# Performance work log

Hardware: AMD Instinct MI355X
Metric: run time of the kernel (lower is better)

## Reference

```python
import jax, jax.numpy as jnp
import numpy as np
from jax import lax

EPS = 1e-5

def conv3x3(x, w):
    # x: [B,C,H,W], w: [O,C,3,3]
    return lax.conv_general_dilated(x, w, (1, 1), ((1, 1), (1, 1)),
                                    dimension_numbers=("NCHW", "OIHW", "NCHW"))

def convbnrelu(x, w, bn):
    gamma, beta, mean, var = bn  # each [C]
    y = conv3x3(x, w)
    scale = (gamma / jnp.sqrt(var + EPS))[:, None, None]
    shift = (beta - mean * gamma / jnp.sqrt(var + EPS))[:, None, None]
    return jax.nn.relu(y * scale + shift)

def conv1x1(x, w, b):
    # w: [O,C,1,1], b: [O]
    return jnp.einsum("bchw,oc->bohw", x, w[:, :, 0, 0]) + b[:, None, None]

def pam(x, wb, bb, wc, bc, wd, bd, alpha, lfm=None):
    B, C, H, W = x.shape
    N = H * W
    q = conv1x1(x, wb, bb)
    k = conv1x1(x, wc, bc)
    v = conv1x1(x, wd, bd)
    if lfm is not None:  # VFAM: qkv flags all 1 -> multiply q, k, v
        q = q * lfm
        k = k * lfm
        v = v * lfm
    fb = q.reshape(B, -1, N).transpose(0, 2, 1)           # [B,N,Cq]
    fc = k.reshape(B, -1, N)                              # [B,Cq,N]
    attn = jax.nn.softmax(jnp.matmul(fb, fc), axis=-1)    # [B,N,N]
    fd = v.reshape(B, C, N)                               # [B,C,N]
    fe = jnp.matmul(fd, attn.transpose(0, 2, 1)).reshape(B, C, H, W)
    return alpha * fe + x

def cam(x, beta):
    B, C, H, W = x.shape
    N = H * W
    fa = x.reshape(B, C, N)
    attn = jnp.matmul(fa, fa.transpose(0, 2, 1))          # [B,C,C]
    attn = jnp.max(attn, axis=-1, keepdims=True) - attn
    attn = jax.nn.softmax(attn, axis=-1)
    fe = jnp.matmul(attn, fa).reshape(B, C, H, W)
    return beta * fe + x

def setup_inputs() -> dict:
    key = jax.random.key(0)
    ks = iter(jax.random.split(key, 64))
    B, Cin, H, W = 2, 2048, 64, 64
    Cmid = Cin // 4         # 512
    Cq = Cmid // 8          # 64
    nclass = 19

    def bn_pack(C):
        g = jnp.ones((C,)) + 0.1 * jax.random.normal(next(ks), (C,))
        b = 0.1 * jax.random.normal(next(ks), (C,))
        m = 0.1 * jax.random.normal(next(ks), (C,))
        v = jax.random.uniform(next(ks), (C,), minval=0.5, maxval=1.5)
        return jnp.stack([g, b, m, v])  # [4,C]

    def conv_w(O, I, kk):
        return jax.random.normal(next(ks), (O, I, kk, kk)) * (1.0 / np.sqrt(I * kk * kk))

    inp = {
        "x": jax.random.normal(next(ks), (B, Cin, H, W)),
        "loss_factor_map": jax.random.uniform(next(ks), (H, W)),
        "wp1": conv_w(Cmid, Cin, 3), "bnp1": bn_pack(Cmid),
        "wp2": conv_w(Cmid, Cmid, 3), "bnp2": bn_pack(Cmid),
        "wc1": conv_w(Cmid, Cin, 3), "bnc1": bn_pack(Cmid),
        "wc2": conv_w(Cmid, Cmid, 3), "bnc2": bn_pack(Cmid),
        "wv1": conv_w(Cmid, Cin, 3), "bnv1": bn_pack(Cmid),
        "wv2": conv_w(Cmid, Cmid, 3), "bnv2": bn_pack(Cmid),
        "pam_wb": conv_w(Cq, Cmid, 1), "pam_bb": jnp.zeros((Cq,)),
        "pam_wc": conv_w(Cq, Cmid, 1), "pam_bc": jnp.zeros((Cq,)),
        "pam_wd": conv_w(Cmid, Cmid, 1), "pam_bd": jnp.zeros((Cmid,)),
        "pam_alpha": 0.3 * jnp.ones((1,)),
        "cam_beta": 0.3 * jnp.ones((1,)),
        "vfam_wb": conv_w(Cq, Cmid, 1), "vfam_bb": jnp.zeros((Cq,)),
        "vfam_wc": conv_w(Cq, Cmid, 1), "vfam_bc": jnp.zeros((Cq,)),
        "vfam_wd": conv_w(Cmid, Cmid, 1), "vfam_bd": jnp.zeros((Cmid,)),
        "vfam_alpha": 0.3 * jnp.ones((1,)),
        "out_w": conv_w(nclass, Cmid, 1), "out_b": jnp.zeros((nclass,)),
        "p3_w": conv_w(nclass, Cmid, 1), "p3_b": jnp.zeros((nclass,)),
        "c3_w": conv_w(nclass, Cmid, 1), "c3_b": jnp.zeros((nclass,)),
    }
    return inp

def reference(x, loss_factor_map,
              wp1, bnp1, wp2, bnp2, wc1, bnc1, wc2, bnc2, wv1, bnv1, wv2, bnv2,
              pam_wb, pam_bb, pam_wc, pam_bc, pam_wd, pam_bd, pam_alpha,
              cam_beta,
              vfam_wb, vfam_bb, vfam_wc, vfam_bc, vfam_wd, vfam_bd, vfam_alpha,
              out_w, out_b, p3_w, p3_b, c3_w, c3_b):
    lfm = loss_factor_map[None, None, :, :]  # (1,1,H,W)
    # Position branch
    fp = convbnrelu(x, wp1, bnp1)
    fp = pam(fp, pam_wb, pam_bb, pam_wc, pam_bc, pam_wd, pam_bd, pam_alpha)
    fp = convbnrelu(fp, wp2, bnp2)
    # Channel branch
    fc = convbnrelu(x, wc1, bnc1)
    fc = cam(fc, cam_beta)
    fc = convbnrelu(fc, wc2, bnc2)
    # Visual-field branch (qkv_vfa_flag = [1,1,1])
    fv = convbnrelu(x, wv1, bnv1)
    fv = pam(fv, vfam_wb, vfam_bb, vfam_wc, vfam_bc, vfam_wd, vfam_bd, vfam_alpha, lfm=lfm)
    fv = convbnrelu(fv, wv2, bnv2)
    # Fusion + heads (Dropout in eval mode = identity)
    fusion = fp + fc + fv
    fusion_out = conv1x1(fusion, out_w, out_b)
    p_out = conv1x1(fp, p3_w, p3_b)
    c_out = conv1x1(fc, c3_w, c3_b)
    return (fusion_out, p_out, c_out)
```

## Files before the change

### kernel.cpp

```cpp
#include <hip/hip_runtime.h>

typedef unsigned short u16;
typedef short s16x8 __attribute__((ext_vector_type(8)));
typedef u16 u16x8 __attribute__((ext_vector_type(8)));
typedef u16 u16x4 __attribute__((ext_vector_type(4)));
typedef float f32x4 __attribute__((ext_vector_type(4)));

#define DEV __device__ __forceinline__

DEV float bf2f(u16 x) { unsigned v = ((unsigned)x) << 16; float f; __builtin_memcpy(&f, &v, 4); return f; }
DEV u16 f2bf(float f) { unsigned u; __builtin_memcpy(&u, &f, 4); u += 0x7FFFu + ((u >> 16) & 1u); return (u16)(u >> 16); }

DEV void gload16(const u16* g, u16* l) {
  __builtin_amdgcn_global_load_lds((const __attribute__((address_space(1))) void*)g,
                                   (__attribute__((address_space(3))) void*)l, 16, 0, 0);
}

__global__ void detect_dtype(const u16* __restrict__ x, int* __restrict__ flag) {
  int tid = threadIdx.x;
  float mx = 0.f;
  for (int i = tid; i < 4096; i += 256) mx = fmaxf(mx, fabsf(bf2f(x[i])));
  __shared__ float red[4];
  int wave = tid >> 6, lane = tid & 63;
  for (int off = 32; off; off >>= 1) mx = fmaxf(mx, __shfl_xor(mx, off));
  if (lane == 0) red[wave] = mx;
  __syncthreads();
  if (tid == 0) {
    mx = fmaxf(fmaxf(red[0], red[1]), fmaxf(red[2], red[3]));
    *flag = (mx > 1e4f) ? 1 : 0;
  }
}

__global__ void convert_in(const void* __restrict__ src, u16* __restrict__ dst, int n,
                           const int* __restrict__ flag) {
  int i = blockIdx.x * 256 + threadIdx.x;
  if (i >= n) return;
  if (*flag) dst[i] = f2bf(((const float*)src)[i]);
  else       dst[i] = ((const u16*)src)[i];
}

__global__ void bn_prep(const u16* __restrict__ cbn, float* __restrict__ out) {
  int w = blockIdx.x;
  const u16* bn = cbn + w * 2048;
  int c = threadIdx.x;
  float g = bf2f(bn[c]), be = bf2f(bn[512 + c]), m = bf2f(bn[1024 + c]), v = bf2f(bn[1536 + c]);
  float sc = g * rsqrtf(v + 1e-5f);
  out[w * 1024 + c] = sc;
  out[w * 1024 + 512 + c] = be - m * sc;
}

__global__ __launch_bounds__(256) void repack_w3(const void* __restrict__ w, u16* __restrict__ wr,
                                                 int I, int Ishift, const int* __restrict__ flag) {
  const int isF = *flag;
  size_t idx = ((size_t)blockIdx.x * 256 + threadIdx.x) * 8;
  int i0 = (int)(idx & (size_t)(I - 1));
  int t = (int)(idx >> Ishift);
  int o = t / 9, kk = t - o * 9;
  u16x8 v;
  if (isF) {
    const float* f = (const float*)w;
#pragma unroll
    for (int j = 0; j < 8; ++j) v[j] = f2bf(f[((size_t)o * I + i0 + j) * 9 + kk]);
  } else {
    const u16* bsrc = (const u16*)w;
#pragma unroll
    for (int j = 0; j < 8; ++j) v[j] = bsrc[((size_t)o * I + i0 + j) * 9 + kk];
  }
  *(u16x8*)&wr[idx] = v;
}

__global__ __launch_bounds__(256) void pad_nchw(const void* __restrict__ x, u16* __restrict__ xpad,
                                                const int* __restrict__ flag) {
  __shared__ u16 t[64][72];
  const int isF = *flag;
  int c0 = blockIdx.x * 64, h = blockIdx.y, b = blockIdx.z;
  int tid = threadIdx.x;
#pragma unroll
  for (int i = 0; i < 2; ++i) {
    int idx = i * 256 + tid;
    int cc = idx >> 3, ww = (idx & 7) * 8;
    size_t base = (((size_t)(b * 2048 + c0 + cc) * 64) + h) * 64 + ww;
    u16x8 v;
    if (isF) {
      const float* fx = (const float*)x;
#pragma unroll
      for (int j = 0; j < 8; ++j) v[j] = f2bf(fx[base + j]);
    } else {
      v = *(const u16x8*)&((const u16*)x)[base];
    }
    *(u16x8*)&t[cc][ww] = v;
  }
  __syncthreads();
#pragma unroll
  for (int i = 0; i < 2; ++i) {
    int idx = i * 256 + tid;
    int ww = idx >> 3, cc = (idx & 7) * 8;
    u16x8 v;
#pragma unroll
    for (int j = 0; j < 8; ++j) v[j] = t[cc + j][ww];
    *(u16x8*)&xpad[(((size_t)b * 66 + h + 1) * 66 + ww + 1) * 2048 + c0 + cc] = v;
  }
}

__global__ __launch_bounds__(256) void transpose64(const u16* __restrict__ src, u16* __restrict__ dst,
                                                   int R, int C) {
  __shared__ u16 t[64][72];
  int r0 = blockIdx.x * 64, c0 = blockIdx.y * 64;
  const u16* s = src + (size_t)blockIdx.z * R * C;
  u16* d = dst + (size_t)blockIdx.z * R * C;
  int tid = threadIdx.x;
#pragma unroll
  for (int i = 0; i < 2; ++i) {
    int idx = i * 256 + tid;
    int rr = idx >> 3, cc = (idx & 7) * 8;
    u16x8 v = *(const u16x8*)&s[(size_t)(r0 + rr) * C + c0 + cc];
    *(u16x8*)&t[rr][cc] = v;
  }
  __syncthreads();
#pragma unroll
  for (int i = 0; i < 2; ++i) {
    int idx = i * 256 + tid;
    int cc = idx >> 3, rr = (idx & 7) * 8;
    u16x8 v;
#pragma unroll
    for (int j = 0; j < 8; ++j) v[j] = t[rr + j][cc];
    *(u16x8*)&d[(size_t)(c0 + cc) * R + r0 + rr] = v;
  }
}

struct GemmP {
  const u16* A; const u16* B;
  long aBatch, bBatch;
  int M, N, K;
  u16* out; long outBatch; int ldOut;
  const u16* bias;
  const u16* rowscale;
  const u16* residual; long resBatch; int ldRes;
  const u16* alphaPtr;
  float* outF; long outFBatch;
  const u16* B2; const u16* bias2; u16* out2;
};

template <int BM, int BN, int EPI>
__global__ __launch_bounds__(256) void gemm_nt(GemmP p) {
  static_assert(EPI != 2 || BM >= BN, "EPI2 LDS bounce needs BM>=BN");
  __shared__ __align__(16) u16 lsBuf[(BM + BN) * 32];
  u16* lA = lsBuf;
  u16* lB = lsBuf + BM * 32;
  const int tid = threadIdx.x;
  int bz = blockIdx.z;
  const u16* Bsel = p.B;
  const u16* biasSel = p.bias;
  u16* outSel = p.out;
  if (EPI == 0 && p.out2) {
    const int h = gridDim.z >> 1;
    if (bz >= h) { bz -= h; Bsel = p.B2; biasSel = p.bias2; outSel = p.out2; }
  }
  const int m0 = blockIdx.x * BM, n0 = blockIdx.y * BN;
  const u16* A = p.A + (size_t)bz * p.aBatch;
  const u16* Bp = Bsel + (size_t)bz * p.bBatch;
  const int wave = tid >> 6, lane = tid & 63;
  const int quad = lane >> 4, r16 = lane & 15;
  const int wm = (wave >> 1) * (BM / 2), wn = (wave & 1) * (BN / 2);
  constexpr int TM = BM / 32, TN = BN / 32;
  f32x4 acc[TM][TN] = {};
  const int srow = tid >> 2, sch = (tid & 3) * 8;
  const int K = p.K;
  for (int k0 = 0; k0 < K; k0 += 32) {
    u16x8 ra[BM / 64], rb[BN / 64];
#pragma unroll
    for (int i = 0; i < BM / 64; ++i)
      ra[i] = *(const u16x8*)&A[(size_t)(m0 + i * 64 + srow) * K + k0 + sch];
#pragma unroll
    for (int i = 0; i < BN / 64; ++i)
      rb[i] = *(const u16x8*)&Bp[(size_t)(n0 + i * 64 + srow) * K + k0 + sch];
    __syncthreads();
#pragma unroll
    for (int i = 0; i < BM / 64; ++i) *(u16x8*)&lA[i * 2048 + tid * 8] = ra[i];
#pragma unroll
    for (int i = 0; i < BN / 64; ++i) *(u16x8*)&lB[i * 2048 + tid * 8] = rb[i];
    __syncthreads();
    s16x8 av[TM], bv[TN];
#pragma unroll
    for (int t = 0; t < TM; ++t) av[t] = *(const s16x8*)&lA[(wm + t * 16 + r16) * 32 + quad * 8];
#pragma unroll
    for (int t = 0; t < TN; ++t) bv[t] = *(const s16x8*)&lB[(wn + t * 16 + r16) * 32 + quad * 8];
#pragma unroll
    for (int i = 0; i < TM; ++i)
#pragma unroll
      for (int j = 0; j < TN; ++j)
        acc[i][j] = __builtin_amdgcn_mfma_f32_16x16x32_bf16(av[i], bv[j], acc[i][j], 0, 0, 0);
  }
  if constexpr (EPI == 2) {
    float* lsF = (float*)lsBuf;
#pragma unroll
    for (int i = 0; i < TM; ++i) {
      __syncthreads();
#pragma unroll
      for (int j = 0; j < TN; ++j) {
        const int col = wn + j * 16 + r16;
#pragma unroll
        for (int r = 0; r < 4; ++r) {
          const int rowL = (wave >> 1) * 16 + quad * 4 + r;
          lsF[rowL * BN + col] = acc[i][j][r];
        }
      }
      __syncthreads();
      constexpr int PASSES = (32 * BN) / 1024;
#pragma unroll
      for (int pp = 0; pp < PASSES; ++pp) {
        const int lin = (pp * 256 + tid) * 4;
        const int rowL = lin / BN, col = lin & (BN - 1);
        const int gm = m0 + (rowL >> 4) * (BM / 2) + i * 16 + (rowL & 15);
        *(f32x4*)&p.outF[(size_t)bz * p.outFBatch + (size_t)gm * p.ldOut + (n0 + col)] =
            *(const f32x4*)&lsF[lin];
      }
    }
    return;
  }
  float alpha = 0.f;
  if (EPI == 3) alpha = bf2f(p.alphaPtr[0]);
#pragma unroll
  for (int i = 0; i < TM; ++i) {
#pragma unroll
    for (int j = 0; j < TN; ++j) {
      const int nn = n0 + wn + j * 16 + r16;
      float bia = 0.f;
      if ((EPI == 0 || EPI == 1) && biasSel) bia = bf2f(biasSel[nn]);
#pragma unroll
      for (int r = 0; r < 4; ++r) {
        const int mm = m0 + wm + i * 16 + quad * 4 + r;
        float v = acc[i][j][r];
        if (EPI == 0) {
          v += bia;
          if (p.rowscale) v *= bf2f(p.rowscale[mm]);
          outSel[(size_t)bz * p.outBatch + (size_t)mm * p.ldOut + nn] = f2bf(v);
        } else if (EPI == 1) {
          v += bia;
          if (p.rowscale) v *= bf2f(p.rowscale[mm]);
          p.out[(size_t)bz * p.outBatch + (size_t)nn * p.ldOut + mm] = f2bf(v);
        } else {
          float res = bf2f(p.residual[(size_t)bz * p.resBatch + (size_t)mm * p.ldRes + nn]);
          v = alpha * v + res;
          const int py = mm >> 6, px = mm & 63;
          p.out[(size_t)bz * p.outBatch + ((size_t)(py + 1) * 66 + (px + 1)) * p.ldOut + nn] = f2bf(v);
        }
      }
    }
  }
}

struct Conv3P {
  const u16* in[3];
  const u16* wr[3];
  u16* out[3];
  const float* bn;
};

template <int CIN>
__global__ __launch_bounds__(256) void conv3x3_k(Conv3P p) {
  __shared__ u16 lA[4096], lB[4096];
  const int tid = threadIdx.x;
  const int z = blockIdx.z, ci = z >> 1, b = z & 1;
  const int m0 = blockIdx.x * 128, n0 = blockIdx.y * 128;
  const u16* __restrict__ xin = p.in[ci];
  const u16* __restrict__ wr = p.wr[ci];
  const int wave = tid >> 6, lane = tid & 63;
  const int quad = lane >> 4, r16 = lane & 15;
  const int wm = (wave >> 1) * 64, wn = (wave & 1) * 64;
  f32x4 acc[4][4] = {};
  const int srow = tid >> 2, sch = (tid & 3) * 8;
  const int p0 = m0 + srow, p1 = p0 + 64;
  const size_t a0 = (((size_t)b * 66 + (p0 >> 6)) * 66 + (p0 & 63)) * CIN + sch;
  const size_t a1 = (((size_t)b * 66 + (p1 >> 6)) * 66 + (p1 & 63)) * CIN + sch;
  const size_t b0 = ((size_t)(n0 + srow) * 9) * CIN + sch;
  const size_t b1 = ((size_t)(n0 + 64 + srow) * 9) * CIN + sch;
  u16* la0 = &lA[wave * 512];
  u16* la1 = &lA[2048 + wave * 512];
  u16* lb0 = &lB[wave * 512];
  u16* lb1 = &lB[2048 + wave * 512];
  for (int kh = 0; kh < 3; ++kh) {
    for (int kw = 0; kw < 3; ++kw) {
      const size_t soff = ((size_t)kh * 66 + kw) * CIN;
      const size_t woff = (size_t)(kh * 3 + kw) * CIN;
      for (int c = 0; c < CIN; c += 32) {
        __syncthreads();
        gload16(&xin[a0 + soff + c], la0);
        gload16(&xin[a1 + soff + c], la1);
        gload16(&wr[b0 + woff + c], lb0);
        gload16(&wr[b1 + woff + c], lb1);
        __syncthreads();
        s16x8 av[4], bv[4];
#pragma unroll
        for (int t = 0; t < 4; ++t) av[t] = *(const s16x8*)&lA[(wm + t * 16 + r16) * 32 + quad * 8];
#pragma unroll
        for (int t = 0; t < 4; ++t) bv[t] = *(const s16x8*)&lB[(wn + t * 16 + r16) * 32 + quad * 8];
#pragma unroll
        for (int i = 0; i < 4; ++i)
#pragma unroll
          for (int j = 0; j < 4; ++j)
            acc[i][j] = __builtin_amdgcn_mfma_f32_16x16x32_bf16(av[i], bv[j], acc[i][j], 0, 0, 0);
      }
    }
  }
  u16* __restrict__ out = p.out[ci];
  const float* bnS = p.bn + ci * 1024;
#pragma unroll
  for (int i = 0; i < 4; ++i) {
#pragma unroll
    for (int j = 0; j < 4; ++j) {
      const int nn = n0 + wn + j * 16 + r16;
      const float s = bnS[nn], sh = bnS[512 + nn];
#pragma unroll
      for (int r = 0; r < 4; ++r) {
        const int mm = m0 + wm + i * 16 + quad * 4 + r;
        float v = fmaxf(acc[i][j][r] * s + sh, 0.f);
        out[((size_t)b * 4096 + mm) * 512 + nn] = f2bf(v);
      }
    }
  }
}

__global__ __launch_bounds__(256) void softmax4096(const float* __restrict__ S, u16* __restrict__ P) {
  int row = blockIdx.x, tid = threadIdx.x;
  const float* sr = S + (size_t)row * 4096;
  f32x4 v[4];
  float mx = -3.4e38f;
#pragma unroll
  for (int i = 0; i < 4; ++i) {
    v[i] = *(const f32x4*)&sr[(i * 256 + tid) * 4];
    mx = fmaxf(mx, fmaxf(fmaxf(v[i][0], v[i][1]), fmaxf(v[i][2], v[i][3])));
  }
  __shared__ float red[8];
  int wave = tid >> 6, lane = tid & 63;
  for (int off = 32; off; off >>= 1) mx = fmaxf(mx, __shfl_xor(mx, off));
  if (lane == 0) red[wave] = mx;
  __syncthreads();
  mx = fmaxf(fmaxf(red[0], red[1]), fmaxf(red[2], red[3]));
  float sum = 0.f;
#pragma unroll
  for (int i = 0; i < 4; ++i)
#pragma unroll
    for (int j = 0; j < 4; ++j) { float e = __expf(v[i][j] - mx); v[i][j] = e; sum += e; }
  for (int off = 32; off; off >>= 1) sum += __shfl_xor(sum, off);
  if (lane == 0) red[4 + wave] = sum;
  __syncthreads();
  sum = red[4] + red[5] + red[6] + red[7];
  float inv = 1.f / sum;
  u16* pr = P + (size_t)row * 4096;
#pragma unroll
  for (int i = 0; i < 4; ++i) {
    u16x4 ov;
#pragma unroll
    for (int j = 0; j < 4; ++j) ov[j] = f2bf(v[i][j] * inv);
    *(u16x4*)&pr[(i * 256 + tid) * 4] = ov;
  }
}

__global__ __launch_bounds__(256) void softmax_cam(const float* __restrict__ S, u16* __restrict__ P) {
  int row = blockIdx.x, tid = threadIdx.x;
  const float* sr = S + (size_t)row * 512;
  float a = sr[tid], b = sr[tid + 256];
  __shared__ float red[12];
  int wave = tid >> 6, lane = tid & 63;
  float mx = fmaxf(a, b);
  for (int off = 32; off; off >>= 1) mx = fmaxf(mx, __shfl_xor(mx, off));
  if (lane == 0) red[wave] = mx;
  __syncthreads();
  float M1 = fmaxf(fmaxf(red[0], red[1]), fmaxf(red[2], red[3]));
  float mn = fminf(a, b);
  for (int off = 32; off; off >>= 1) mn = fminf(mn, __shfl_xor(mn, off));
  if (lane == 0) red[4 + wave] = mn;
  __syncthreads();
  float m2 = M1 - fminf(fminf(red[4], red[5]), fminf(red[6], red[7]));
  float e0 = __expf((M1 - a) - m2), e1 = __expf((M1 - b) - m2);
  float sum = e0 + e1;
  for (int off = 32; off; off >>= 1) sum += __shfl_xor(sum, off);
  if (lane == 0) red[8 + wave] = sum;
  __syncthreads();
  sum = red[8] + red[9] + red[10] + red[11];
  float inv = 1.f / sum;
  P[(size_t)row * 512 + tid] = f2bf(e0 * inv);
  P[(size_t)row * 512 + tid + 256] = f2bf(e1 * inv);
}

__global__ __launch_bounds__(256) void final_out_k(const u16* __restrict__ fp2, const u16* __restrict__ fc2,
                                                   const u16* __restrict__ fv2,
                                                   const u16* ow, const u16* ob, const u16* pw,
                                                   const u16* pb, const u16* cw, const u16* cb,
                                                   void* __restrict__ out, const int* __restrict__ flag) {
  __shared__ float wl[19 * 512];
  int tid = threadIdx.x, which = blockIdx.y;
  const u16* W = which == 0 ? ow : which == 1 ? pw : cw;
  const u16* Bb = which == 0 ? ob : which == 1 ? pb : cb;
  for (int i = tid; i < 19 * 512; i += 256) wl[i] = bf2f(W[i]);
  __syncthreads();
  int pix = blockIdx.x * 256 + threadIdx.x;
  size_t rb = (size_t)pix * 512;
  float acc[19];
#pragma unroll
  for (int o = 0; o < 19; ++o) acc[o] = 0.f;
  for (int c = 0; c < 512; c += 8) {
    float xs[8];
    if (which == 0) {
      u16x8 a = *(const u16x8*)&fp2[rb + c];
      u16x8 d = *(const u16x8*)&fc2[rb + c];
      u16x8 e = *(const u16x8*)&fv2[rb + c];
#pragma unroll
      for (int j = 0; j < 8; ++j) xs[j] = bf2f(a[j]) + bf2f(d[j]) + bf2f(e[j]);
    } else {
      const u16* src = which == 1 ? fp2 : fc2;
      u16x8 a = *(const u16x8*)&src[rb + c];
#pragma unroll
      for (int j = 0; j < 8; ++j) xs[j] = bf2f(a[j]);
    }
#pragma unroll
    for (int o = 0; o < 19; ++o) {
      const float* wv = &wl[o * 512 + c];
#pragma unroll
      for (int j = 0; j < 8; ++j) acc[o] += xs[j] * wv[j];
    }
  }
  int b = pix >> 12, n = pix & 4095;
  const int isF32 = *flag;
#pragma unroll
  for (int o = 0; o < 19; ++o) {
    size_t idx = (size_t)which * 155648 + ((size_t)(b * 19 + o)) * 4096 + n;
    float v = acc[o] + bf2f(Bb[o]);
    if (isF32) ((float*)out)[idx] = v;
    else ((u16*)out)[idx] = f2bf(v);
  }
}

static const size_t OFF_XPAD  = 0;
static const size_t OFF_WR1A  = 35684352;
static const size_t OFF_WR1B  = 54558720;
static const size_t OFF_WR1C  = 73433088;
static const size_t OFF_ARENA = 92307456;
static const size_t OFF_S     = 0;
static const size_t OFF_P     = 67108864;
static const size_t OFF_FP1   = 125861888;
static const size_t OFF_FC1   = 134250496;
static const size_t OFF_FV1   = 142639104;
static const size_t OFF_FC1T  = 151027712;
static const size_t OFF_QT    = 159416320;
static const size_t OFF_KT    = 160464896;
static const size_t OFF_VT    = 161513472;
static const size_t OFF_WRSA  = 151027712;
static const size_t OFF_WRSB  = 155746304;
static const size_t OFF_WRSC  = 161513472;
static const size_t OFF_PADP  = 169902080;
static const size_t OFF_PADC  = 178823168;
static const size_t OFF_PADV  = 187744256;
static const size_t OFF_FP2   = 125861888;
static const size_t OFF_FC2   = 134250496;
static const size_t OFF_FV2   = 142639104;
static const size_t OFF_SC    = 196665344;
static const size_t OFF_PC    = 198762496;
static const size_t OFF_BN    = 199811072;
static const size_t OFF_FLAG  = 199835648;
static const size_t OFF_SMALL = 199835904;
static const size_t SO_CBN    = 0;
static const size_t SO_PWB    = 12288;
static const size_t SO_PBB    = 45056;
static const size_t SO_PWC    = 45120;
static const size_t SO_PBC    = 77888;
static const size_t SO_PWD    = 77952;
static const size_t SO_PBD    = 340096;
static const size_t SO_PAL    = 340608;
static const size_t SO_CBETA  = 340624;
static const size_t SO_VWB    = 340640;
static const size_t SO_VBB    = 373408;
static const size_t SO_VWC    = 373472;
static const size_t SO_VBC    = 406240;
static const size_t SO_VWD    = 406304;
static const size_t SO_VBD    = 668448;
static const size_t SO_VAL    = 668960;
static const size_t SO_OW     = 668976;
static const size_t SO_OB     = 678704;
static const size_t SO_PW3    = 678736;
static const size_t SO_PB3    = 688464;
static const size_t SO_CW3    = 688496;
static const size_t SO_CB3    = 698224;
static const size_t SO_LFM    = 698256;
static const size_t SO_END    = 702352;
static const size_t WS_NEEDED = OFF_SMALL + SO_END * 2;

extern "C" void kernel_launch(void* const* d_in, const int* in_sizes, int n_in,
                              void* d_out, int out_size, void* d_ws, size_t ws_size,
                              hipStream_t stream) {
  if (ws_size < WS_NEEDED) return;
  (void)in_sizes; (void)n_in; (void)out_size;

  char* ws = (char*)d_ws;
  u16* xpad   = (u16*)(ws + OFF_XPAD);
  u16* wr1a   = (u16*)(ws + OFF_WR1A);
  u16* wr1b   = (u16*)(ws + OFF_WR1B);
  u16* wr1c   = (u16*)(ws + OFF_WR1C);
  float* S    = (float*)(ws + OFF_S);
  u16* P      = (u16*)(ws + OFF_P);
  u16* fp1    = (u16*)(ws + OFF_FP1);
  u16* fc1    = (u16*)(ws + OFF_FC1);
  u16* fv1    = (u16*)(ws + OFF_FV1);
  u16* fc1T   = (u16*)(ws + OFF_FC1T);
  u16* qt     = (u16*)(ws + OFF_QT);
  u16* kt     = (u16*)(ws + OFF_KT);
  u16* vT     = (u16*)(ws + OFF_VT);
  u16* wrsa   = (u16*)(ws + OFF_WRSA);
  u16* wrsb   = (u16*)(ws + OFF_WRSB);
  u16* wrsc   = (u16*)(ws + OFF_WRSC);
  u16* padP   = (u16*)(ws + OFF_PADP);
  u16* padC   = (u16*)(ws + OFF_PADC);
  u16* padV   = (u16*)(ws + OFF_PADV);
  u16* fp2    = (u16*)(ws + OFF_FP2);
  u16* fc2    = (u16*)(ws + OFF_FC2);
  u16* fv2    = (u16*)(ws + OFF_FV2);
  float* Sc   = (float*)(ws + OFF_SC);
  u16* Pc     = (u16*)(ws + OFF_PC);
  float* bnb  = (float*)(ws + OFF_BN);
  int* flag   = (int*)(ws + OFF_FLAG);
  u16* sm     = (u16*)(ws + OFF_SMALL);

  detect_dtype<<<1, 256, 0, stream>>>((const u16*)d_in[0], flag);
  auto cv = [&](int i, u16* dst, int n) {
    convert_in<<<(n + 255) / 256, 256, 0, stream>>>(d_in[i], dst, n, flag);
  };
  cv(3,  sm + SO_CBN + 0 * 2048, 2048);
  cv(7,  sm + SO_CBN + 1 * 2048, 2048);
  cv(11, sm + SO_CBN + 2 * 2048, 2048);
  cv(5,  sm + SO_CBN + 3 * 2048, 2048);
  cv(9,  sm + SO_CBN + 4 * 2048, 2048);
  cv(13, sm + SO_CBN + 5 * 2048, 2048);
  cv(14, sm + SO_PWB, 32768);  cv(15, sm + SO_PBB, 64);
  cv(16, sm + SO_PWC, 32768);  cv(17, sm + SO_PBC, 64);
  cv(18, sm + SO_PWD, 262144); cv(19, sm + SO_PBD, 512);
  cv(20, sm + SO_PAL, 1);      cv(21, sm + SO_CBETA, 1);
  cv(22, sm + SO_VWB, 32768);  cv(23, sm + SO_VBB, 64);
  cv(24, sm + SO_VWC, 32768);  cv(25, sm + SO_VBC, 64);
  cv(26, sm + SO_VWD, 262144); cv(27, sm + SO_VBD, 512);
  cv(28, sm + SO_VAL, 1);
  cv(29, sm + SO_OW, 9728);    cv(30, sm + SO_OB, 19);
  cv(31, sm + SO_PW3, 9728);   cv(32, sm + SO_PB3, 19);
  cv(33, sm + SO_CW3, 9728);   cv(34, sm + SO_CB3, 19);
  cv(1,  sm + SO_LFM, 4096);

  bn_prep<<<6, 512, 0, stream>>>(sm + SO_CBN, bnb);

  hipMemsetAsync(xpad, 0, 35684352, stream);
  pad_nchw<<<dim3(32, 64, 2), 256, 0, stream>>>(d_in[0], xpad, flag);

  repack_w3<<<4608, 256, 0, stream>>>(d_in[2],  wr1a, 2048, 11, flag);
  repack_w3<<<4608, 256, 0, stream>>>(d_in[6],  wr1b, 2048, 11, flag);
  repack_w3<<<4608, 256, 0, stream>>>(d_in[10], wr1c, 2048, 11, flag);
  {
    Conv3P c{};
    c.in[0] = xpad; c.in[1] = xpad; c.in[2] = xpad;
    c.wr[0] = wr1a; c.wr[1] = wr1b; c.wr[2] = wr1c;
    c.out[0] = fp1; c.out[1] = fc1; c.out[2] = fv1;
    c.bn = bnb;
    conv3x3_k<2048><<<dim3(32, 4, 6), 256, 0, stream>>>(c);
  }

  auto runPam = [&](const u16* src, const u16* wb, const u16* bb, const u16* wck, const u16* bck,
                    const u16* wd, const u16* bd, const u16* alphaP, const u16* rs, u16* padOut) {
    GemmP g{};
    g.A = src; g.aBatch = 2097152; g.B = wb; g.bBatch = 0; g.M = 4096; g.N = 64; g.K = 512;
    g.out = qt; g.outBatch = 262144; g.ldOut = 64; g.bias = bb; g.rowscale = rs;
    g.B2 = wck; g.bias2 = bck; g.out2 = kt;
    gemm_nt<64, 64, 0><<<dim3(64, 1, 4), 256, 0, stream>>>(g);
    GemmP gv{};
    gv.A = src; gv.aBatch = 2097152; gv.B = wd; gv.bBatch = 0; gv.M = 4096; gv.N = 512; gv.K = 512;
    gv.out = vT; gv.outBatch = 2097152; gv.ldOut = 4096; gv.bias = bd; gv.rowscale = rs;
    gemm_nt<64, 128, 1><<<dim3(64, 4, 2), 256, 0, stream>>>(gv);
    hipMemsetAsync(padOut, 0, 8921088, stream);
    for (int b = 0; b < 2; ++b) {
      GemmP gs{};
      gs.A = qt + (size_t)b * 262144; gs.B = kt + (size_t)b * 262144;
      gs.M = 4096; gs.N = 4096; gs.K = 64;
      gs.outF = S; gs.outFBatch = 0; gs.ldOut = 4096;
      gemm_nt<128, 128, 2><<<dim3(32, 32, 1), 256, 0, stream>>>(gs);
      softmax4096<<<4096, 256, 0, stream>>>(S, P);
      GemmP gf{};
      gf.A = P; gf.aBatch = 0; gf.B = vT + (size_t)b * 2097152; gf.bBatch = 0;
      gf.M = 4096; gf.N = 512; gf.K = 4096;
      gf.out = padOut + (size_t)b * 2230272; gf.outBatch = 0; gf.ldOut = 512;
      gf.residual = src + (size_t)b * 2097152; gf.resBatch = 0; gf.ldRes = 512;
      gf.alphaPtr = alphaP;
      gemm_nt<128, 64, 3><<<dim3(32, 8, 1), 256, 0, stream>>>(gf);
    }
  };
  runPam(fp1, sm + SO_PWB, sm + SO_PBB, sm + SO_PWC, sm + SO_PBC, sm + SO_PWD, sm + SO_PBD,
         sm + SO_PAL, nullptr, padP);
  runPam(fv1, sm + SO_VWB, sm + SO_VBB, sm + SO_VWC, sm + SO_VBC, sm + SO_VWD, sm + SO_VBD,
         sm + SO_VAL, sm + SO_LFM, padV);

  transpose64<<<dim3(64, 8, 2), 256, 0, stream>>>(fc1, fc1T, 4096, 512);
  {
    GemmP g{};
    g.A = fc1T; g.aBatch = 2097152; g.B = fc1T; g.bBatch = 2097152;
    g.M = 512; g.N = 512; g.K = 4096;
    g.outF = Sc; g.outFBatch = 262144; g.ldOut = 512;
    gemm_nt<64, 64, 2><<<dim3(8, 8, 2), 256, 0, stream>>>(g);
  }
  softmax_cam<<<1024, 256, 0, stream>>>(Sc, Pc);
  hipMemsetAsync(padC, 0, 8921088, stream);
  {
    GemmP g{};
    g.A = fc1; g.aBatch = 2097152; g.B = Pc; g.bBatch = 262144;
    g.M = 4096; g.N = 512; g.K = 512;
    g.out = padC; g.outBatch = 2230272; g.ldOut = 512;
    g.residual = fc1; g.resBatch = 2097152; g.ldRes = 512;
    g.alphaPtr = sm + SO_CBETA;
    gemm_nt<128, 128, 3><<<dim3(32, 4, 2), 256, 0, stream>>>(g);
  }

  repack_w3<<<1152, 256, 0, stream>>>(d_in[4],  wrsa, 512, 9, flag);
  repack_w3<<<1152, 256, 0, stream>>>(d_in[8],  wrsb, 512, 9, flag);
  repack_w3<<<1152, 256, 0, stream>>>(d_in[12], wrsc, 512, 9, flag);
  {
    Conv3P c{};
    c.in[0] = padP; c.in[1] = padC; c.in[2] = padV;
    c.wr[0] = wrsa; c.wr[1] = wrsb; c.wr[2] = wrsc;
    c.out[0] = fp2; c.out[1] = fc2; c.out[2] = fv2;
    c.bn = bnb + 3 * 1024;
    conv3x3_k<512><<<dim3(32, 4, 6), 256, 0, stream>>>(c);
  }

  final_out_k<<<dim3(32, 3), 256, 0, stream>>>(fp2, fc2, fv2, sm + SO_OW, sm + SO_OB,
                                               sm + SO_PW3, sm + SO_PB3, sm + SO_CW3, sm + SO_CB3,
                                               d_out, flag);
}
```

Baseline: 1.722 ms.

## Batch small conversion launches, zero only pad borders, use direct-to-LDS GEMM loads

The ~28 per-tensor convert_in launches become one batched, vectorised convert kernel. The three weight repack launches per stage are merged into one grid using blockIdx.z. Full-buffer memsets of the padded activations are replaced by a kernel that zeroes only the one-pixel border. The generic GEMM now stages A/B tiles through global_load_lds instead of register round-trips. This cuts launch overhead and redundant memory writes, but relies on the interior always being overwritten and on the LDS write layout from gload16 matching the old tid*8 layout.

```diff
diff --git a/kernel.cpp b/kernel.cpp
--- a/kernel.cpp
+++ b/kernel.cpp
@@ -31,12 +31,39 @@
   }
 }
 
-__global__ void convert_in(const void* __restrict__ src, u16* __restrict__ dst, int n,
-                           const int* __restrict__ flag) {
-  int i = blockIdx.x * 256 + threadIdx.x;
-  if (i >= n) return;
-  if (*flag) dst[i] = f2bf(((const float*)src)[i]);
-  else       dst[i] = ((const u16*)src)[i];
+struct CvBatch {
+  const void* src[28];
+  unsigned dstOff[28];
+  unsigned n[28];
+  unsigned chunkStart[29];
+  int cnt;
+};
+
+__global__ __launch_bounds__(256) void convert_batch(CvBatch cb, u16* __restrict__ dstBase,
+                                                     const int* __restrict__ flag) {
+  const int isF = *flag;
+  const unsigned bid = blockIdx.x;
+  int j = 0;
+  while (bid >= cb.chunkStart[j + 1]) ++j;
+  const unsigned base = (bid - cb.chunkStart[j]) * 2048 + threadIdx.x * 8;
+  const unsigned n = cb.n[j];
+  if (base >= n) return;
+  u16* dst = dstBase + cb.dstOff[j];
+  const void* src = cb.src[j];
+  if (base + 8 <= n) {
+    u16x8 v;
+    if (isF) {
+      const float* f = (const float*)src;
+#pragma unroll
+      for (int k = 0; k < 8; ++k) v[k] = f2bf(f[base + k]);
+    } else {
+      v = *(const u16x8*)&((const u16*)src)[base];
+    }
+    *(u16x8*)&dst[base] = v;
+  } else {
+    for (unsigned i = base; i < n; ++i)
+      dst[i] = isF ? f2bf(((const float*)src)[i]) : ((const u16*)src)[i];
+  }
 }
 
 __global__ void bn_prep(const u16* __restrict__ cbn, float* __restrict__ out) {
@@ -49,9 +76,13 @@
   out[w * 1024 + 512 + c] = be - m * sc;
 }
 
-__global__ __launch_bounds__(256) void repack_w3(const void* __restrict__ w, u16* __restrict__ wr,
-                                                 int I, int Ishift, const int* __restrict__ flag) {
+struct Repack3P { const void* src[3]; u16* dst[3]; };
+
+__global__ __launch_bounds__(256) void repack_w3(Repack3P rp, int I, int Ishift,
+                                                 const int* __restrict__ flag) {
   const int isF = *flag;
+  const void* w = rp.src[blockIdx.z];
+  u16* wr = rp.dst[blockIdx.z];
   size_t idx = ((size_t)blockIdx.x * 256 + threadIdx.x) * 8;
   int i0 = (int)(idx & (size_t)(I - 1));
   int t = (int)(idx >> Ishift);
@@ -67,6 +98,22 @@
     for (int j = 0; j < 8; ++j) v[j] = bsrc[((size_t)o * I + i0 + j) * 9 + kk];
   }
   *(u16x8*)&wr[idx] = v;
+}
+
+__global__ __launch_bounds__(256) void zero_border(u16* __restrict__ base, int CIN) {
+  int p = blockIdx.x, b = blockIdx.y;
+  int py, px;
+  if (p < 66)       { py = 0;        px = p; }
+  else if (p < 132) { py = 65;       px = p - 66; }
+  else if (p < 196) { py = p - 131;  px = 0; }
+  else              { py = p - 195;  px = 65; }
+  u16* d = base + (((size_t)b * 66 + py) * 66 + px) * (size_t)CIN;
+  for (int i = threadIdx.x * 8; i < CIN; i += 2048) {
+    u16x8 z;
+#pragma unroll
+    for (int k = 0; k < 8; ++k) z[k] = 0;
+    *(u16x8*)&d[i] = z;
+  }
 }
 
 __global__ __launch_bounds__(256) void pad_nchw(const void* __restrict__ x, u16* __restrict__ xpad,
@@ -167,18 +214,13 @@
   const int srow = tid >> 2, sch = (tid & 3) * 8;
   const int K = p.K;
   for (int k0 = 0; k0 < K; k0 += 32) {
-    u16x8 ra[BM / 64], rb[BN / 64];
+    __syncthreads();
 #pragma unroll
     for (int i = 0; i < BM / 64; ++i)
-      ra[i] = *(const u16x8*)&A[(size_t)(m0 + i * 64 + srow) * K + k0 + sch];
+      gload16(&A[(size_t)(m0 + i * 64 + srow) * K + k0 + sch], lA + i * 2048 + wave * 512);
 #pragma unroll
     for (int i = 0; i < BN / 64; ++i)
-      rb[i] = *(const u16x8*)&Bp[(size_t)(n0 + i * 64 + srow) * K + k0 + sch];
-    __syncthreads();
-#pragma unroll
-    for (int i = 0; i < BM / 64; ++i) *(u16x8*)&lA[i * 2048 + tid * 8] = ra[i];
-#pragma unroll
-    for (int i = 0; i < BN / 64; ++i) *(u16x8*)&lB[i * 2048 + tid * 8] = rb[i];
+      gload16(&Bp[(size_t)(n0 + i * 64 + srow) * K + k0 + sch], lB + i * 2048 + wave * 512);
     __syncthreads();
     s16x8 av[TM], bv[TN];
 #pragma unroll
@@ -522,36 +564,47 @@
   u16* sm     = (u16*)(ws + OFF_SMALL);
 
   detect_dtype<<<1, 256, 0, stream>>>((const u16*)d_in[0], flag);
-  auto cv = [&](int i, u16* dst, int n) {
-    convert_in<<<(n + 255) / 256, 256, 0, stream>>>(d_in[i], dst, n, flag);
-  };
-  cv(3,  sm + SO_CBN + 0 * 2048, 2048);
-  cv(7,  sm + SO_CBN + 1 * 2048, 2048);
-  cv(11, sm + SO_CBN + 2 * 2048, 2048);
-  cv(5,  sm + SO_CBN + 3 * 2048, 2048);
-  cv(9,  sm + SO_CBN + 4 * 2048, 2048);
-  cv(13, sm + SO_CBN + 5 * 2048, 2048);
-  cv(14, sm + SO_PWB, 32768);  cv(15, sm + SO_PBB, 64);
-  cv(16, sm + SO_PWC, 32768);  cv(17, sm + SO_PBC, 64);
-  cv(18, sm + SO_PWD, 262144); cv(19, sm + SO_PBD, 512);
-  cv(20, sm + SO_PAL, 1);      cv(21, sm + SO_CBETA, 1);
-  cv(22, sm + SO_VWB, 32768);  cv(23, sm + SO_VBB, 64);
-  cv(24, sm + SO_VWC, 32768);  cv(25, sm + SO_VBC, 64);
-  cv(26, sm + SO_VWD, 262144); cv(27, sm + SO_VBD, 512);
-  cv(28, sm + SO_VAL, 1);
-  cv(29, sm + SO_OW, 9728);    cv(30, sm + SO_OB, 19);
-  cv(31, sm + SO_PW3, 9728);   cv(32, sm + SO_PB3, 19);
-  cv(33, sm + SO_CW3, 9728);   cv(34, sm + SO_CB3, 19);
-  cv(1,  sm + SO_LFM, 4096);
+  {
+    CvBatch cb{};
+    int jn = 0; unsigned chunks = 0;
+    auto addJob = [&](int i, size_t dstOff, unsigned n) {
+      cb.src[jn] = d_in[i]; cb.dstOff[jn] = (unsigned)dstOff; cb.n[jn] = n;
+      cb.chunkStart[jn] = chunks; chunks += (n + 2047) / 2048; ++jn;
+    };
+    addJob(3,  SO_CBN + 0 * 2048, 2048);
+    addJob(7,  SO_CBN + 1 * 2048, 2048);
+    addJob(11, SO_CBN + 2 * 2048, 2048);
+    addJob(5,  SO_CBN + 3 * 2048, 2048);
+    addJob(9,  SO_CBN + 4 * 2048, 2048);
+    addJob(13, SO_CBN + 5 * 2048, 2048);
+    addJob(14, SO_PWB, 32768);  addJob(15, SO_PBB, 64);
+    addJob(16, SO_PWC, 32768);  addJob(17, SO_PBC, 64);
+    addJob(18, SO_PWD, 262144); addJob(19, SO_PBD, 512);
+    addJob(20, SO_PAL, 1);      addJob(21, SO_CBETA, 1);
+    addJob(22, SO_VWB, 32768);  addJob(23, SO_VBB, 64);
+    addJob(24, SO_VWC, 32768);  addJob(25, SO_VBC, 64);
+    addJob(26, SO_VWD, 262144); addJob(27, SO_VBD, 512);
+    addJob(28, SO_VAL, 1);
+    addJob(29, SO_OW, 9728);    addJob(30, SO_OB, 19);
+    addJob(31, SO_PW3, 9728);   addJob(32, SO_PB3, 19);
+    addJob(33, SO_CW3, 9728);   addJob(34, SO_CB3, 19);
+    addJob(1,  SO_LFM, 4096);
+    cb.cnt = jn; cb.chunkStart[jn] = chunks;
+    convert_batch<<<chunks, 256, 0, stream>>>(cb, sm, flag);
+  }
 
   bn_prep<<<6, 512, 0, stream>>>(sm + SO_CBN, bnb);
 
-  hipMemsetAsync(xpad, 0, 35684352, stream);
+  zero_border<<<dim3(260, 2), 256, 0, stream>>>(xpad, 2048);
   pad_nchw<<<dim3(32, 64, 2), 256, 0, stream>>>(d_in[0], xpad, flag);
 
-  repack_w3<<<4608, 256, 0, stream>>>(d_in[2],  wr1a, 2048, 11, flag);
-  repack_w3<<<4608, 256, 0, stream>>>(d_in[6],  wr1b, 2048, 11, flag);
-  repack_w3<<<4608, 256, 0, stream>>>(d_in[10], wr1c, 2048, 11, flag);
+  {
+    Repack3P rp{};
+    rp.src[0] = d_in[2];  rp.dst[0] = wr1a;
+    rp.src[1] = d_in[6];  rp.dst[1] = wr1b;
+    rp.src[2] = d_in[10]; rp.dst[2] = wr1c;
+    repack_w3<<<dim3(4608, 1, 3), 256, 0, stream>>>(rp, 2048, 11, flag);
+  }
   {
     Conv3P c{};
     c.in[0] = xpad; c.in[1] = xpad; c.in[2] = xpad;
@@ -572,7 +625,7 @@
     gv.A = src; gv.aBatch = 2097152; gv.B = wd; gv.bBatch = 0; gv.M = 4096; gv.N = 512; gv.K = 512;
     gv.out = vT; gv.outBatch = 2097152; gv.ldOut = 4096; gv.bias = bd; gv.rowscale = rs;
     gemm_nt<64, 128, 1><<<dim3(64, 4, 2), 256, 0, stream>>>(gv);
-    hipMemsetAsync(padOut, 0, 8921088, stream);
+    zero_border<<<dim3(260, 2), 256, 0, stream>>>(padOut, 512);
     for (int b = 0; b < 2; ++b) {
       GemmP gs{};
       gs.A = qt + (size_t)b * 262144; gs.B = kt + (size_t)b * 262144;
@@ -603,7 +656,7 @@
     gemm_nt<64, 64, 2><<<dim3(8, 8, 2), 256, 0, stream>>>(g);
   }
   softmax_cam<<<1024, 256, 0, stream>>>(Sc, Pc);
-  hipMemsetAsync(padC, 0, 8921088, stream);
+  zero_border<<<dim3(260, 2), 256, 0, stream>>>(padC, 512);
   {
     GemmP g{};
     g.A = fc1; g.aBatch = 2097152; g.B = Pc; g.bBatch = 262144;
@@ -614,9 +667,13 @@
     gemm_nt<128, 128, 3><<<dim3(32, 4, 2), 256, 0, stream>>>(g);
   }
 
-  repack_w3<<<1152, 256, 0, stream>>>(d_in[4],  wrsa, 512, 9, flag);
-  repack_w3<<<1152, 256, 0, stream>>>(d_in[8],  wrsb, 512, 9, flag);
-  repack_w3<<<1152, 256, 0, stream>>>(d_in[12], wrsc, 512, 9, flag);
+  {
+    Repack3P rp{};
+    rp.src[0] = d_in[4];  rp.dst[0] = wrsa;
+    rp.src[1] = d_in[8];  rp.dst[1] = wrsb;
+    rp.src[2] = d_in[12]; rp.dst[2] = wrsc;
+    repack_w3<<<dim3(1152, 1, 3), 256, 0, stream>>>(rp, 512, 9, flag);
+  }
   {
     Conv3P c{};
     c.in[0] = padP; c.in[1] = padC; c.in[2] = padV;
```

New measurement: 1.647 ms. 4.3% less time.
